# Performance work log

Hardware: AMD Instinct MI355X
Metric: run time of the kernel (lower is better)

## Reference

```python
import jax, jax.numpy as jnp
import numpy as np

N = 50000        # nodes
E = 800000       # edges (avg degree 16)
HID = 96         # hidden_channels
HEADS = 4        # heads passed to SRGATConv
D = HID // HEADS # per-head dim
R = 38           # num_relations
NEG_SLOPE = 0.2  # LeakyReLU slope for attention logits


def setup_inputs() -> dict:
    key = jax.random.key(0)
    ks = jax.random.split(key, 9)
    x = jax.random.normal(ks[0], (N, HID), jnp.float32)
    edge_index = jax.random.randint(ks[1], (2, E), 0, N, dtype=jnp.int32)
    edge_type = jax.random.randint(ks[2], (E,), 0, R, dtype=jnp.int32)
    s = 1.0 / np.sqrt(HID)
    W = jax.random.normal(ks[3], (HID, HID), jnp.float32) * s          # node projection
    rel_emb = jax.random.normal(ks[4], (R, HID), jnp.float32) * s      # relation embeddings
    att_src = jax.random.normal(ks[5], (HEADS, D), jnp.float32) * 0.1  # attention vectors
    att_dst = jax.random.normal(ks[6], (HEADS, D), jnp.float32) * 0.1
    att_rel = jax.random.normal(ks[7], (HEADS, D), jnp.float32) * 0.1
    bias = jnp.zeros((HID,), jnp.float32)
    return {"x": x, "edge_index": edge_index, "edge_type": edge_type,
            "W": W, "rel_emb": rel_emb, "att_src": att_src,
            "att_dst": att_dst, "att_rel": att_rel, "bias": bias}


def reference(x, edge_index, edge_type, W, rel_emb, att_src, att_dst, att_rel, bias):
    # SRGATConv: relation-aware multi-head graph attention, then GELU wrapper.
    n = x.shape[0]
    src, dst = edge_index[0], edge_index[1]
    h = (x @ W).reshape(n, HEADS, D)                    # [N,H,D]
    r = rel_emb[edge_type].reshape(-1, HEADS, D)        # [E,H,D] gathered relation feats
    h_src = h[src]                                      # [E,H,D] irregular gather
    h_dst = h[dst]
    # attention logits per edge/head
    logits = ((h_src * att_src).sum(-1)
              + (h_dst * att_dst).sum(-1)
              + (r * att_rel).sum(-1))                  # [E,H]
    logits = jax.nn.leaky_relu(logits, NEG_SLOPE)
    # segment softmax over incoming edges of each destination node
    lmax = jax.ops.segment_max(logits, dst, num_segments=n)   # [N,H]
    e = jnp.exp(logits - lmax[dst])
    denom = jax.ops.segment_sum(e, dst, num_segments=n)       # [N,H]
    alpha = e / denom[dst]                                    # [E,H]
    # weighted message scatter
    msg = alpha[:, :, None] * (h_src + r)                     # [E,H,D]
    out = jax.ops.segment_sum(msg, dst, num_segments=n).reshape(n, HID) + bias
    out = jax.nn.gelu(out)
    return out, alpha
```

## Files before the change

### kernel.cpp

```cpp
#include <hip/hip_runtime.h>
#include <hip/hip_fp16.h>
#include <math.h>

#define HIDC 96
#define HEADS 4
#define RMAX 40
#define BINSZ 64
#define BINB 6
#define BINCAP 1344
#define TILE 2048
#define SRCB 18
#define SRCM ((1 << SRCB) - 1)
#define ETB 6
#define NBMAX 1024

typedef unsigned u32x2 __attribute__((ext_vector_type(2)));
typedef _Float16 f16x4 __attribute__((ext_vector_type(4)));
typedef float f32x4 __attribute__((ext_vector_type(4)));

__device__ __forceinline__ __half2 u2h2(unsigned u) {
    return *reinterpret_cast<__half2*>(&u);
}
__device__ __forceinline__ unsigned h22u(__half2 h) {
    return *reinterpret_cast<unsigned*>(&h);
}

__global__ __launch_bounds__(256) void gemm96(const float* __restrict__ x,
                                              const float* __restrict__ W,
                                              __half* __restrict__ h16,
                                              int* __restrict__ bincnt,
                                              int4* __restrict__ csrtail,
                                              int n, int nbins) {
    for (int i = blockIdx.x * 256 + threadIdx.x; i < nbins; i += gridDim.x * 256)
        bincnt[i] = 0;
    if (blockIdx.x == 0 && threadIdx.x < 16)
        csrtail[threadIdx.x] = make_int4(0, 0, 0, 0);

    const int lane = threadIdx.x & 63;
    const int wave = threadIdx.x >> 6;
    const int lo16 = lane & 15;
    const int grp = lane >> 4;

    f16x4 bf[6][6];
#pragma unroll
    for (int kf = 0; kf < 6; ++kf)
#pragma unroll
        for (int nt = 0; nt < 6; ++nt) {
            f16x4 b;
#pragma unroll
            for (int j = 0; j < 4; ++j)
                b[j] = (_Float16)W[(kf * 16 + grp * 4 + j) * HIDC + nt * 16 + lo16];
            bf[kf][nt] = b;
        }

    int row0 = blockIdx.x * 64 + wave * 16;
    if (row0 >= n) return;
    int r = row0 + lo16;
    const float4* xr = reinterpret_cast<const float4*>(
        x + (size_t)min(r, n - 1) * HIDC);

    f32x4 c[6];
#pragma unroll
    for (int nt = 0; nt < 6; ++nt) c[nt] = (f32x4){0.f, 0.f, 0.f, 0.f};

#pragma unroll
    for (int kf = 0; kf < 6; ++kf) {
        float4 av = xr[kf * 4 + grp];
        f16x4 af;
        af[0] = (_Float16)av.x; af[1] = (_Float16)av.y;
        af[2] = (_Float16)av.z; af[3] = (_Float16)av.w;
#pragma unroll
        for (int nt = 0; nt < 6; ++nt)
            c[nt] = __builtin_amdgcn_mfma_f32_16x16x16f16(af, bf[kf][nt], c[nt], 0, 0, 0);
    }

#pragma unroll
    for (int nt = 0; nt < 6; ++nt)
#pragma unroll
        for (int i = 0; i < 4; ++i) {
            int rr = row0 + grp * 4 + i;
            if (rr < n)
                h16[(size_t)rr * HIDC + nt * 16 + lo16] = (__half)c[nt][i];
        }
}

__global__ __launch_bounds__(256) void node_dots(
    const __half* __restrict__ h16,
    const float* __restrict__ att_src, const float* __restrict__ att_dst,
    const float* __restrict__ rel, const float* __restrict__ att_rel,
    float4* __restrict__ ps, float* __restrict__ pdi,
    float4* __restrict__ pr, int n, int R_) {
    if (blockIdx.x == gridDim.x - 1) {
        int t = threadIdx.x;
        if (t < R_) {
            const float4* rp = reinterpret_cast<const float4*>(rel + (size_t)t * HIDC);
            const float4* ar = reinterpret_cast<const float4*>(att_rel);
            float acc[HEADS] = {0, 0, 0, 0};
#pragma unroll
            for (int c = 0; c < 24; ++c) {
                float4 v = rp[c], a = ar[c];
                acc[c / 6] += v.x * a.x + v.y * a.y + v.z * a.z + v.w * a.w;
            }
            pr[t] = make_float4(acc[0], acc[1], acc[2], acc[3]);
        }
        return;
    }
    int i = blockIdx.x * blockDim.x + threadIdx.x;
    if (i >= n) return;
    const uint2* hp = reinterpret_cast<const uint2*>(h16 + (size_t)i * HIDC);
    const float4* as = reinterpret_cast<const float4*>(att_src);
    const float4* ad = reinterpret_cast<const float4*>(att_dst);
    float accs[HEADS] = {0, 0, 0, 0}, accd[HEADS] = {0, 0, 0, 0};
#pragma unroll
    for (int c = 0; c < 24; ++c) {
        uint2 hv = hp[c];
        float2 f0 = __half22float2(u2h2(hv.x));
        float2 f1 = __half22float2(u2h2(hv.y));
        float4 a = as[c], d = ad[c];
        int hh = c / 6;
        accs[hh] += f0.x * a.x + f0.y * a.y + f1.x * a.z + f1.y * a.w;
        accd[hh] += f0.x * d.x + f0.y * d.y + f1.x * d.z + f1.y * d.w;
    }
    ps[i] = make_float4(accs[0], accs[1], accs[2], accs[3]);
    *reinterpret_cast<float4*>(pdi + (size_t)i * 8) =
        make_float4(accd[0], accd[1], accd[2], accd[3]);
}

__device__ __forceinline__ float4 ev4(float4 a, float4 b, float4 c) {
    float l0 = a.x + b.x + c.x, l1 = a.y + b.y + c.y;
    float l2 = a.z + b.z + c.z, l3 = a.w + b.w + c.w;
    l0 = l0 >= 0.f ? l0 : 0.2f * l0;
    l1 = l1 >= 0.f ? l1 : 0.2f * l1;
    l2 = l2 >= 0.f ? l2 : 0.2f * l2;
    l3 = l3 >= 0.f ? l3 : 0.2f * l3;
    return make_float4(__expf(l0), __expf(l1), __expf(l2), __expf(l3));
}

__device__ __forceinline__ float gelu_f(float v) {
    float u = 0.7978845608028654f * (v + 0.044715f * v * v * v);
    u = fminf(fmaxf(u, -15.f), 15.f);
    float t = __expf(2.f * u);
    return 0.5f * v * (1.f + (t - 1.f) / (t + 1.f));
}

__global__ __launch_bounds__(256) void bin_edges(
    const int* __restrict__ src, const int* __restrict__ dst,
    const int* __restrict__ et,
    int* __restrict__ bincnt, int2* __restrict__ binwords,
    int E_, int nbins) {
    __shared__ int hist[NBMAX];
    __shared__ int base[NBMAX];
    int e0 = blockIdx.x * TILE;
    for (int i = threadIdx.x; i < nbins; i += 256) hist[i] = 0;
    __syncthreads();
    int mybin[8], myrank[8], myword[8];
#pragma unroll
    for (int u = 0; u < 8; ++u) {
        int e = e0 + u * 256 + threadIdx.x;
        mybin[u] = -1;
        if (e < E_) {
            int d = dst[e];
            int b = d >> BINB;
            myword[u] = src[e] | (et[e] << SRCB) | ((d & (BINSZ - 1)) << (SRCB + ETB));
            mybin[u] = b;
            myrank[u] = atomicAdd(&hist[b], 1);
        }
    }
    __syncthreads();
    for (int i = threadIdx.x; i < nbins; i += 256)
        base[i] = hist[i] > 0 ? atomicAdd(&bincnt[i], hist[i]) : 0;
    __syncthreads();
#pragma unroll
    for (int u = 0; u < 8; ++u) {
        if (mybin[u] >= 0) {
            int pos = base[mybin[u]] + myrank[u];
            if (pos < BINCAP)
                binwords[(size_t)mybin[u] * BINCAP + pos] =
                    make_int2(myword[u], e0 + u * 256 + threadIdx.x);
        }
    }
}

__global__ __launch_bounds__(256) void bin_sort(
    const int* __restrict__ bincnt, const int2* __restrict__ binwords,
    const float4* __restrict__ ps, const float* __restrict__ pdi,
    const float4* __restrict__ prg,
    int4* __restrict__ csr, int* __restrict__ noff, int* __restrict__ ncnt,
    int n, int R_) {
    __shared__ int cnts[BINSZ];
    __shared__ int scanb[BINSZ];
    __shared__ int nbase[BINSZ];
    __shared__ float4 pdl[BINSZ];
    __shared__ float4 prl[RMAX];
    int bin = blockIdx.x;
    int node0 = bin * BINSZ;
    int total = min(bincnt[bin], BINCAP);

    for (int i = threadIdx.x; i < BINSZ; i += 256) {
        cnts[i] = 0;
        int nd = node0 + i;
        pdl[i] = (nd < n) ? *reinterpret_cast<const float4*>(pdi + (size_t)nd * 8)
                          : make_float4(0.f, 0.f, 0.f, 0.f);
    }
    for (int i = threadIdx.x; i < R_; i += 256) prl[i] = prg[i];
    __syncthreads();

    int2 w[6];
    int rk[6];
    float4 psv[6];
#pragma unroll
    for (int u = 0; u < 6; ++u) {
        int k = u * 256 + threadIdx.x;
        rk[u] = -1;
        if (k < total) {
            w[u] = binwords[(size_t)bin * BINCAP + k];
            psv[u] = ps[w[u].x & SRCM];
            int dl = (w[u].x >> (SRCB + ETB)) & (BINSZ - 1);
            rk[u] = atomicAdd(&cnts[dl], 1);
        }
    }
    __syncthreads();

    if (threadIdx.x < BINSZ) scanb[threadIdx.x] = (cnts[threadIdx.x] + 3) & ~3;
    __syncthreads();
    for (int s = 1; s < BINSZ; s <<= 1) {
        int v = 0;
        if (threadIdx.x < BINSZ && threadIdx.x >= s) v = scanb[threadIdx.x - s];
        __syncthreads();
        if (threadIdx.x < BINSZ) scanb[threadIdx.x] += v;
        __syncthreads();
    }
    if (threadIdx.x < BINSZ) {
        int cnt = cnts[threadIdx.x];
        int cntP = (cnt + 3) & ~3;
        int nb = scanb[threadIdx.x] - cntP;
        nbase[threadIdx.x] = nb;
        int nd = node0 + threadIdx.x;
        if (nd < n) {
            noff[nd] = bin * BINCAP + nb;
            ncnt[nd] = cnt;
        }
        int4 z = make_int4(0, 0, 0, 0);
        for (int i = cnt; i < cntP; ++i)
            csr[(size_t)bin * BINCAP + nb + i] = z;
    }
    {
        int gt = scanb[BINSZ - 1];
        if (threadIdx.x < 12) {
            int p = gt + threadIdx.x;
            if (p < BINCAP)
                csr[(size_t)bin * BINCAP + p] = make_int4(0, 0, 0, 0);
        }
    }
    __syncthreads();

#pragma unroll
    for (int u = 0; u < 6; ++u) {
        if (rk[u] >= 0) {
            int s = w[u].x & SRCM;
            int t = (w[u].x >> SRCB) & ((1 << ETB) - 1);
            int dl = (w[u].x >> (SRCB + ETB)) & (BINSZ - 1);
            unsigned e = (unsigned)w[u].y;
            float4 v = ev4(psv[u], pdl[dl], prl[t]);
            int4 pk;
            pk.x = (int)((unsigned)(s * (HIDC * 2)) | ((e & 0xFFu) << 24));
            pk.y = (int)((unsigned)(t * (HIDC * 2)) | ((e >> 8) << 13));
            pk.z = (int)h22u(__floats2half2_rn(v.x, v.y));
            pk.w = (int)h22u(__floats2half2_rn(v.z, v.w));
            csr[(size_t)bin * BINCAP + nbase[dl] + rk[u]] = pk;
        }
    }
}

__global__ __launch_bounds__(256) void node_agg(
    const __half* __restrict__ h16, const float* __restrict__ rel,
    const int4* __restrict__ csr, const int* __restrict__ noff,
    const int* __restrict__ ncnt,
    const float* __restrict__ bias,
    float* __restrict__ out, float4* __restrict__ alpha, int n, int R_) {
    __shared__ uint2 relh[RMAX * HIDC / 4];
    for (int i = threadIdx.x; i < R_ * 24; i += 256) {
        float4 v = reinterpret_cast<const float4*>(rel)[i];
        uint2 pk;
        pk.x = h22u(__floats2half2_rn(v.x, v.y));
        pk.y = h22u(__floats2half2_rn(v.z, v.w));
        relh[i] = pk;
    }
    __syncthreads();

    int lane = threadIdx.x & 31;
    if (lane >= 24) return;
    const int j = lane;
    const int j4 = 4 * j;
    const int hh = j / 6;
    const unsigned joff = (unsigned)(j << 3);
    const float4 bv = *reinterpret_cast<const float4*>(bias + j4);
    const char* h16c = reinterpret_cast<const char*>(h16);
    const char* relc = reinterpret_cast<const char*>(relh);
    const unsigned esel = (unsigned)(2 * hh) | ((unsigned)(2 * hh + 1) << 8);

    int hw0 = (blockIdx.x * blockDim.x + threadIdx.x) >> 5;
    int nHW = (gridDim.x * blockDim.x) >> 5;

    for (int hw = hw0; hw < n; hw += nHW) {
        int cnt = ncnt[hw];
        const int4* sp0 = csr + noff[hw];
        const int4* sp = sp0;
        float a0 = 0.f, a1 = 0.f, a2 = 0.f, a3 = 0.f;
        float dsum = 0.f;

        if (cnt > 0) {
            int cntP = (cnt + 3) & ~3;
            int4 pc[4];
#pragma unroll
            for (int u = 0; u < 4; ++u) pc[u] = sp[u];
            sp += 4;

            for (int k = 0; k < cntP; k += 4, sp += 4) {
                uint2 hv[4], rv[4];
#pragma unroll
                for (int u = 0; u < 4; ++u)
                    hv[u] = *reinterpret_cast<const uint2*>(
                        h16c + ((unsigned)pc[u].x & 0x00FFFFFFu) + joff);
#pragma unroll
                for (int u = 0; u < 4; ++u)
                    rv[u] = *reinterpret_cast<const uint2*>(
                        relc + ((unsigned)pc[u].y & 0x1FFFu) + joff);
                int4 pn[4];
#pragma unroll
                for (int u = 0; u < 4; ++u) pn[u] = sp[u];
#pragma unroll
                for (int u = 0; u < 4; ++u) {
                    unsigned e32 = __builtin_amdgcn_perm(
                        (unsigned)pc[u].w, (unsigned)pc[u].z, esel);
                    dsum += __half2float(__low2half(u2h2(e32)));
                    unsigned s01 = h22u(__hadd2(u2h2(hv[u].x), u2h2(rv[u].x)));
                    unsigned s23 = h22u(__hadd2(u2h2(hv[u].y), u2h2(rv[u].y)));
                    asm("v_fma_mix_f32 %0, %1, %2, %0 op_sel:[0,0,0] op_sel_hi:[1,1,0]"
                        : "+v"(a0) : "v"(s01), "v"(e32));
                    asm("v_fma_mix_f32 %0, %1, %2, %0 op_sel:[1,0,0] op_sel_hi:[1,1,0]"
                        : "+v"(a1) : "v"(s01), "v"(e32));
                    asm("v_fma_mix_f32 %0, %1, %2, %0 op_sel:[0,0,0] op_sel_hi:[1,1,0]"
                        : "+v"(a2) : "v"(s23), "v"(e32));
                    asm("v_fma_mix_f32 %0, %1, %2, %0 op_sel:[1,0,0] op_sel_hi:[1,1,0]"
                        : "+v"(a3) : "v"(s23), "v"(e32));
                }
#pragma unroll
                for (int u = 0; u < 4; ++u) pc[u] = pn[u];
            }
        }
        float inv = dsum > 0.f ? 1.f / dsum : 0.f;
        float4 o;
        o.x = gelu_f(a0 * inv + bv.x);
        o.y = gelu_f(a1 * inv + bv.y);
        o.z = gelu_f(a2 * inv + bv.z);
        o.w = gelu_f(a3 * inv + bv.w);
        *reinterpret_cast<float4*>(out + (size_t)hw * HIDC + j4) = o;

        if (cnt > 0) {
            float iv0 = __shfl(inv, 0, 32);
            float iv1 = __shfl(inv, 6, 32);
            float iv2 = __shfl(inv, 12, 32);
            float iv3 = __shfl(inv, 18, 32);
            for (int k = j; k < cnt; k += 24) {
                int4 pk = sp0[k];
                unsigned e_id = ((unsigned)pk.x >> 24) | (((unsigned)pk.y >> 13) << 8);
                float2 f01 = __half22float2(u2h2((unsigned)pk.z));
                float2 f23 = __half22float2(u2h2((unsigned)pk.w));
                alpha[e_id] = make_float4(f01.x * iv0, f01.y * iv1,
                                          f23.x * iv2, f23.y * iv3);
            }
        }
    }
}

extern "C" void kernel_launch(void* const* d_in, const int* in_sizes, int n_in,
                              void* d_out, int out_size, void* d_ws, size_t ws_size,
                              hipStream_t stream) {
    const float* x       = (const float*)d_in[0];
    const int*   eidx    = (const int*)d_in[1];
    const int*   etype   = (const int*)d_in[2];
    const float* W       = (const float*)d_in[3];
    const float* rel     = (const float*)d_in[4];
    const float* att_src = (const float*)d_in[5];
    const float* att_dst = (const float*)d_in[6];
    const float* att_rel = (const float*)d_in[7];
    const float* bias    = (const float*)d_in[8];

    int N_ = in_sizes[0] / HIDC;
    int E_ = in_sizes[1] / 2;
    int R_ = in_sizes[4] / HIDC;
    const int* src  = eidx;
    const int* dstp = eidx + E_;
    int nbins = (N_ + BINSZ - 1) / BINSZ;

    char* ws = (char*)d_ws;
    __half* h16      = (__half*)ws; ws += (size_t)N_ * HIDC * 2;
    float4* ps       = (float4*)ws; ws += (size_t)N_ * 16;
    float*  pdi      = (float*)ws;  ws += (size_t)N_ * 32;
    float4* pr       = (float4*)ws; ws += 1024;
    int*    bincnt   = (int*)ws;    ws += (size_t)((nbins + 3) & ~3) * 4;
    int*    noff     = (int*)ws;    ws += (size_t)((N_ + 3) & ~3) * 4;
    int*    ncnt     = (int*)ws;    ws += (size_t)((N_ + 3) & ~3) * 4;
    int2*   binwords = (int2*)ws;   ws += (size_t)nbins * BINCAP * 8;
    int4*   csr      = (int4*)ws;   ws += (size_t)nbins * BINCAP * 16 + 256;

    float*  outv  = (float*)d_out;
    float4* alpha = (float4*)(outv + (size_t)N_ * HIDC);

    gemm96<<<(N_ + 63) / 64, 256, 0, stream>>>(
        x, W, h16, bincnt, csr + (size_t)nbins * BINCAP, N_, nbins);

    node_dots<<<(N_ + 255) / 256 + 1, 256, 0, stream>>>(
        h16, att_src, att_dst, rel, att_rel, ps, pdi, pr, N_, R_);

    bin_edges<<<(E_ + TILE - 1) / TILE, 256, 0, stream>>>(
        src, dstp, etype, bincnt, binwords, E_, nbins);

    bin_sort<<<nbins, 256, 0, stream>>>(
        bincnt, binwords, ps, pdi, pr, csr, noff, ncnt, N_, R_);

    node_agg<<<(N_ + 15) / 16, 256, 0, stream>>>(
        h16, rel, csr, noff, ncnt, bias, outv, alpha, N_, R_);
}
```

Before: 177.4 us.

## Fuse node attention dots into GEMM epilogue and use wave-shuffle scan in bin_sort

Removes the separate node_dots kernel. The per-node source/destination attention dot products are now computed directly from the MFMA accumulators in the gemm96 epilogue, using cross-lane shuffle reductions, and the relation dot products are computed in block 0. This saves a kernel launch and a re-read of h16 from memory. The values now come from fp32 accumulators instead of rounded fp16, which slightly changes numerics. Separately, the LDS Hillis-Steele scan in bin_sort is replaced by a single-wave __shfl_up scan, which removes many __syncthreads.

```diff
diff --git a/kernel.cpp b/kernel.cpp
--- a/kernel.cpp
+++ b/kernel.cpp
@@ -25,16 +25,30 @@
     return *reinterpret_cast<unsigned*>(&h);
 }
 
-__global__ __launch_bounds__(256) void gemm96(const float* __restrict__ x,
-                                              const float* __restrict__ W,
-                                              __half* __restrict__ h16,
-                                              int* __restrict__ bincnt,
-                                              int4* __restrict__ csrtail,
-                                              int n, int nbins) {
+__global__ __launch_bounds__(256) void gemm96(
+    const float* __restrict__ x, const float* __restrict__ W,
+    const float* __restrict__ att_src, const float* __restrict__ att_dst,
+    const float* __restrict__ rel, const float* __restrict__ att_rel,
+    __half* __restrict__ h16, float4* __restrict__ ps,
+    float* __restrict__ pdi, float4* __restrict__ pr,
+    int* __restrict__ bincnt, int4* __restrict__ csrtail,
+    int n, int nbins, int R_) {
     for (int i = blockIdx.x * 256 + threadIdx.x; i < nbins; i += gridDim.x * 256)
         bincnt[i] = 0;
     if (blockIdx.x == 0 && threadIdx.x < 16)
         csrtail[threadIdx.x] = make_int4(0, 0, 0, 0);
+    if (blockIdx.x == 0 && threadIdx.x < R_) {
+        int t = threadIdx.x;
+        const float4* rp = reinterpret_cast<const float4*>(rel + (size_t)t * HIDC);
+        const float4* ar = reinterpret_cast<const float4*>(att_rel);
+        float acc[HEADS] = {0, 0, 0, 0};
+#pragma unroll
+        for (int c = 0; c < 24; ++c) {
+            float4 v = rp[c], a = ar[c];
+            acc[c / 6] += v.x * a.x + v.y * a.y + v.z * a.z + v.w * a.w;
+        }
+        pr[t] = make_float4(acc[0], acc[1], acc[2], acc[3]);
+    }
 
     const int lane = threadIdx.x & 63;
     const int wave = threadIdx.x >> 6;
@@ -82,48 +96,64 @@
             if (rr < n)
                 h16[(size_t)rr * HIDC + nt * 16 + lo16] = (__half)c[nt][i];
         }
-}
-
-__global__ __launch_bounds__(256) void node_dots(
-    const __half* __restrict__ h16,
-    const float* __restrict__ att_src, const float* __restrict__ att_dst,
-    const float* __restrict__ rel, const float* __restrict__ att_rel,
-    float4* __restrict__ ps, float* __restrict__ pdi,
-    float4* __restrict__ pr, int n, int R_) {
-    if (blockIdx.x == gridDim.x - 1) {
-        int t = threadIdx.x;
-        if (t < R_) {
-            const float4* rp = reinterpret_cast<const float4*>(rel + (size_t)t * HIDC);
-            const float4* ar = reinterpret_cast<const float4*>(att_rel);
-            float acc[HEADS] = {0, 0, 0, 0};
-#pragma unroll
-            for (int c = 0; c < 24; ++c) {
-                float4 v = rp[c], a = ar[c];
-                acc[c / 6] += v.x * a.x + v.y * a.y + v.z * a.z + v.w * a.w;
+
+    float as_[6], ad_[6];
+#pragma unroll
+    for (int nt = 0; nt < 6; ++nt) {
+        as_[nt] = att_src[nt * 16 + lo16];
+        ad_[nt] = att_dst[nt * 16 + lo16];
+    }
+    bool lo8 = lo16 < 8;
+    float a1lo = lo8 ? as_[1] : 0.f, a1hi = lo8 ? 0.f : as_[1];
+    float d1lo = lo8 ? ad_[1] : 0.f, d1hi = lo8 ? 0.f : ad_[1];
+    float a4lo = lo8 ? as_[4] : 0.f, a4hi = lo8 ? 0.f : as_[4];
+    float d4lo = lo8 ? ad_[4] : 0.f, d4hi = lo8 ? 0.f : ad_[4];
+
+    float sA[4][4], sD[4][4];
+#pragma unroll
+    for (int i = 0; i < 4; ++i) {
+        float v0 = c[0][i], v1 = c[1][i], v2 = c[2][i];
+        float v3 = c[3][i], v4 = c[4][i], v5 = c[5][i];
+        sA[i][0] = v0 * as_[0] + v1 * a1lo;
+        sA[i][1] = v1 * a1hi + v2 * as_[2];
+        sA[i][2] = v3 * as_[3] + v4 * a4lo;
+        sA[i][3] = v4 * a4hi + v5 * as_[5];
+        sD[i][0] = v0 * ad_[0] + v1 * d1lo;
+        sD[i][1] = v1 * d1hi + v2 * ad_[2];
+        sD[i][2] = v3 * ad_[3] + v4 * d4lo;
+        sD[i][3] = v4 * d4hi + v5 * ad_[5];
+    }
+#pragma unroll
+    for (int i = 0; i < 4; ++i)
+#pragma unroll
+        for (int h = 0; h < 4; ++h) {
+#pragma unroll
+            for (int m = 1; m < 16; m <<= 1) {
+                sA[i][h] += __shfl_xor(sA[i][h], m);
+                sD[i][h] += __shfl_xor(sD[i][h], m);
             }
-            pr[t] = make_float4(acc[0], acc[1], acc[2], acc[3]);
-        }
-        return;
-    }
-    int i = blockIdx.x * blockDim.x + threadIdx.x;
-    if (i >= n) return;
-    const uint2* hp = reinterpret_cast<const uint2*>(h16 + (size_t)i * HIDC);
-    const float4* as = reinterpret_cast<const float4*>(att_src);
-    const float4* ad = reinterpret_cast<const float4*>(att_dst);
-    float accs[HEADS] = {0, 0, 0, 0}, accd[HEADS] = {0, 0, 0, 0};
-#pragma unroll
-    for (int c = 0; c < 24; ++c) {
-        uint2 hv = hp[c];
-        float2 f0 = __half22float2(u2h2(hv.x));
-        float2 f1 = __half22float2(u2h2(hv.y));
-        float4 a = as[c], d = ad[c];
-        int hh = c / 6;
-        accs[hh] += f0.x * a.x + f0.y * a.y + f1.x * a.z + f1.y * a.w;
-        accd[hh] += f0.x * d.x + f0.y * d.y + f1.x * d.z + f1.y * d.w;
-    }
-    ps[i] = make_float4(accs[0], accs[1], accs[2], accs[3]);
-    *reinterpret_cast<float4*>(pdi + (size_t)i * 8) =
-        make_float4(accd[0], accd[1], accd[2], accd[3]);
+        }
+    {
+        int rr = row0 + grp * 4 + lo16;
+        if (lo16 < 4 && rr < n) {
+            float4 pv, dv;
+            if (lo16 == 0) {
+                pv = make_float4(sA[0][0], sA[0][1], sA[0][2], sA[0][3]);
+                dv = make_float4(sD[0][0], sD[0][1], sD[0][2], sD[0][3]);
+            } else if (lo16 == 1) {
+                pv = make_float4(sA[1][0], sA[1][1], sA[1][2], sA[1][3]);
+                dv = make_float4(sD[1][0], sD[1][1], sD[1][2], sD[1][3]);
+            } else if (lo16 == 2) {
+                pv = make_float4(sA[2][0], sA[2][1], sA[2][2], sA[2][3]);
+                dv = make_float4(sD[2][0], sD[2][1], sD[2][2], sD[2][3]);
+            } else {
+                pv = make_float4(sA[3][0], sA[3][1], sA[3][2], sA[3][3]);
+                dv = make_float4(sD[3][0], sD[3][1], sD[3][2], sD[3][3]);
+            }
+            ps[rr] = pv;
+            *reinterpret_cast<float4*>(pdi + (size_t)rr * 8) = dv;
+        }
+    }
 }
 
 __device__ __forceinline__ float4 ev4(float4 a, float4 b, float4 c) {
@@ -221,15 +251,16 @@
     }
     __syncthreads();
 
-    if (threadIdx.x < BINSZ) scanb[threadIdx.x] = (cnts[threadIdx.x] + 3) & ~3;
-    __syncthreads();
-    for (int s = 1; s < BINSZ; s <<= 1) {
-        int v = 0;
-        if (threadIdx.x < BINSZ && threadIdx.x >= s) v = scanb[threadIdx.x - s];
-        __syncthreads();
-        if (threadIdx.x < BINSZ) scanb[threadIdx.x] += v;
-        __syncthreads();
-    }
+    if (threadIdx.x < 64) {
+        int v = (cnts[threadIdx.x] + 3) & ~3;
+#pragma unroll
+        for (int s = 1; s < 64; s <<= 1) {
+            int t = __shfl_up(v, s, 64);
+            if ((int)threadIdx.x >= s) v += t;
+        }
+        scanb[threadIdx.x] = v;
+    }
+    __syncthreads();
     if (threadIdx.x < BINSZ) {
         int cnt = cnts[threadIdx.x];
         int cntP = (cnt + 3) & ~3;
@@ -409,10 +440,8 @@
     float4* alpha = (float4*)(outv + (size_t)N_ * HIDC);
 
     gemm96<<<(N_ + 63) / 64, 256, 0, stream>>>(
-        x, W, h16, bincnt, csr + (size_t)nbins * BINCAP, N_, nbins);
-
-    node_dots<<<(N_ + 255) / 256 + 1, 256, 0, stream>>>(
-        h16, att_src, att_dst, rel, att_rel, ps, pdi, pr, N_, R_);
+        x, W, att_src, att_dst, rel, att_rel, h16, ps, pdi, pr,
+        bincnt, csr + (size_t)nbins * BINCAP, N_, nbins, R_);
 
     bin_edges<<<(E_ + TILE - 1) / TILE, 256, 0, stream>>>(
         src, dstp, etype, bincnt, binwords, E_, nbins);
```

Result: faster. 172.8 us (-2.6%).
